# Kernel optimization log

Hardware: AMD Instinct MI355X
Metric: run time of the kernel (lower is better)

Reference implementation:

```python
import jax, jax.numpy as jnp
import numpy as np

B = 32768
PASSES = 4

# mask layout: (batch, digit, row, col), values in {0,1}

def _to_lines(m, d):
    """Reorder so the last axis enumerates the 9 cells of a line and axis -2 the 9 lines."""
    if d == 'h':
        return m                      # lines = rows, cells = cols
    if d == 'v':
        return jnp.swapaxes(m, 2, 3)  # lines = cols, cells = rows
    b = m.shape[0]                    # lines = 3x3 boxes
    return m.reshape(b, 9, 3, 3, 3, 3).transpose(0, 1, 2, 4, 3, 5).reshape(b, 9, 9, 9)

_from_lines = _to_lines  # all three reorderings are self-inverse


def filter_line(m, d):
    """SudokuFilterHVBox: remove a solved cell's digit from all other cells in its line."""
    l = _to_lines(m, d)
    cnt = l.sum(axis=1, keepdims=True)                 # candidates per cell
    solved = l * (cnt == 1).astype(l.dtype)            # one-hot solved cells
    other = solved.sum(axis=-1, keepdims=True) - solved  # same digit solved elsewhere in line
    out = l * (other == 0).astype(l.dtype)
    return _from_lines(out, d)


def unique_line(m, d):
    """SudokuUniqueHVBox (hidden single): if a digit fits only one cell in a line, fix it."""
    l = _to_lines(m, d)
    cnt_line = l.sum(axis=-1, keepdims=True)           # per-digit count in the line
    hidden = l * (cnt_line == 1).astype(l.dtype)       # lone placements
    has = hidden.sum(axis=1, keepdims=True) > 0        # cell hosts a hidden single
    out = jnp.where(has, hidden, l)
    return _from_lines(out, d)


def doubles_line(m, d):
    """SudokuDigitsDoubles (naked pair): two identical 2-candidate cells in a line
    eliminate those digits from the rest of the line."""
    l = _to_lines(m, d)                                # (B, d, line, cell)
    cnt = l.sum(axis=1, keepdims=True)
    pm = l * (cnt == 2).astype(l.dtype)                # patterns of 2-candidate cells
    dot = jnp.einsum('bdlc,bdle->blce', pm, pm)        # pattern overlap between cells
    eye = jnp.eye(9, dtype=l.dtype)
    match = (dot == 2).astype(l.dtype) * (1.0 - eye)   # identical pair at another cell
    pairflag = match.sum(-1) > 0                       # (B, line, cell) part of a naked pair
    pair_digit = pm * pairflag[:, None, :, :].astype(l.dtype)
    total_pd = pair_digit.sum(-1, keepdims=True)       # digit belongs to some pair in line
    remove = (total_pd > 0) & (pair_digit == 0)
    out = l * (1.0 - remove.astype(l.dtype))
    return _from_lines(out, d)


def pointing(m, d):
    """SudokuDigitsInOneLineAtBox: if a digit's box candidates lie in one row/col,
    remove that digit from the rest of the row/col outside the box."""
    b = m.shape[0]
    v = m.reshape(b, 9, 3, 3, 3, 3)                    # (B, d, br, ri, bc, ci)
    if d == 'h':
        pres = v.sum(axis=5) > 0                       # (B,d,br,ri,bc) digit in row of box
        nrows = pres.sum(axis=3, keepdims=True)
        point = pres & (nrows == 1)                    # confined to single row within box
        tot = point.sum(axis=4, keepdims=True)         # over bc
        rem = (tot - point) > 0                        # pointing from another box hits us
        out = v * (1.0 - rem[..., None].astype(v.dtype))
    else:
        pres = v.sum(axis=3) > 0                       # (B,d,br,bc,ci) digit in col of box
        ncols = pres.sum(axis=4, keepdims=True)
        point = pres & (ncols == 1)
        tot = point.sum(axis=2, keepdims=True)         # over br
        rem = (tot - point) > 0
        out = v * (1.0 - rem[:, :, :, None, :, :].astype(v.dtype))
    return out.reshape(b, 9, 9, 9)


def _forward_mask(mask):
    for _ in range(PASSES):
        mask = filter_line(mask, 'box')
        mask = pointing(mask, 'h')
        mask = pointing(mask, 'v')
        mask = unique_line(mask, 'h')
        mask = unique_line(mask, 'v')
        mask = unique_line(mask, 'box')
        mask = doubles_line(mask, 'v')   # original code instantiates doubles_h with 'v'
        mask = doubles_line(mask, 'v')
        mask = doubles_line(mask, 'box')
    return mask


def setup_inputs() -> dict:
    key = jax.random.key(0)
    mask = jax.random.randint(key, (B, 9, 9, 9), 0, 2).astype(jnp.float32)
    return {"mask": mask}


def reference(mask):
    out = _forward_mask(mask)
    cnt = out.sum(axis=1)                              # candidates per cell
    solved = jnp.all(cnt == 1, axis=(1, 2))            # (B,) puzzle fully determined
    return (out, solved)
```

## Files before the change

### kernel.cpp

```cpp
#include <hip/hip_runtime.h>
#include <stdint.h>

#define NB 32768
#define NPASS 4
#define FULL27 0x07FFFFFFu
#define NWORDS (NB * 27)


__global__ __launch_bounds__(256)
void pack_kernel(const uint32_t* __restrict__ in, uint32_t* __restrict__ packed) {
    __shared__ uint32_t pool[4][56];
    const int lane = threadIdx.x & 63;
    const int wv = threadIdx.x >> 6;
    const size_t wordBase = (size_t)blockIdx.x * 256 + (size_t)wv * 64;
    const uint32_t* src = in + wordBase * 27;
    #pragma unroll
    for (int i = 0; i < 27; ++i) {
        uint32_t v = src[(size_t)i * 64 + lane];
        unsigned long long m = __ballot(v != 0u);
        if (lane == 0) {
            pool[wv][2 * i]     = (uint32_t)m;
            pool[wv][2 * i + 1] = (uint32_t)(m >> 32);
        }
    }
    __syncthreads();
    const int bit = lane * 27;
    const int di = bit >> 5;
    uint64_t both = (uint64_t)pool[wv][di] | ((uint64_t)pool[wv][di + 1] << 32);
    packed[wordBase + lane] = (uint32_t)(both >> (bit & 31)) & FULL27;
}

__device__ __forceinline__ uint32_t colfold(uint32_t w) {
    return (w | (w >> 9) | (w >> 18)) & 0x1FFu;
}
__device__ __forceinline__ uint32_t colmaj2(uint32_t w) {
    return ((w & (w >> 9)) | ((w | (w >> 9)) & (w >> 18))) & 0x1FFu;
}

__global__ __launch_bounds__(192, 1)
void solve_kernel(const uint32_t* __restrict__ pin, uint32_t* __restrict__ pout,
                  float* __restrict__ solved) {
    __shared__ uint32_t exA[3][36][64];
    __shared__ uint32_t exB[3][9][64];
    const int lane = threadIdx.x & 63;
    const int band = threadIdx.x >> 6;
    const int bo1 = band == 2 ? 0 : band + 1;
    const int bo2 = band == 0 ? 2 : band - 1;
    const int p = blockIdx.x * 64 + lane;

    uint32_t bd[9];
    {
        const uint32_t* src = pin + (size_t)p * 27 + band;
        #pragma unroll
        for (int d = 0; d < 9; ++d) bd[d] = src[d * 3];
    }

    #pragma unroll 1
    for (int pass = 0; pass < NPASS; ++pass) {
        {
            uint32_t on = 0, tw = 0, fo = 0;
            #pragma unroll
            for (int d = 0; d < 9; ++d) {
                uint32_t c = on & bd[d];
                on ^= bd[d]; fo |= tw & c; tw ^= c;
            }
            uint32_t ex1 = on & ~tw & ~fo;
            #pragma unroll
            for (int d = 0; d < 9; ++d) {
                uint32_t s = bd[d] & ex1;
                #pragma unroll
                for (int k = 0; k < 3; ++k) {
                    uint32_t bm = 0x1C0E07u << (3 * k);
                    uint32_t sm = s & bm;
                    uint32_t multi = sm & (sm - 1u);
                    uint32_t keep = (sm == 0u) ? 0xFFFFFFFFu : (~bm | (multi ? 0u : sm));
                    bd[d] &= keep;
                }
            }
        }

        #pragma unroll
        for (int d = 0; d < 9; ++d) {
            uint32_t w = bd[d];
            uint32_t t = (w | (w >> 1) | (w >> 2)) & 0x01249249u;
            uint32_t sum = (t & 0x1FFu) + ((t >> 9) & 0x1FFu) + ((t >> 18) & 0x1FFu);
            uint32_t single = sum & ~(sum >> 1) & 0x49u;
            uint32_t point = t & (single * 0x40201u);
            uint32_t clearm = 0;
            #pragma unroll
            for (int r = 0; r < 3; ++r) {
                uint32_t pr = (point >> (9 * r)) & 0x1FFu;
                uint32_t multi = pr & (pr - 1u);
                uint32_t segkeep = multi ? 0u : pr * 7u;
                uint32_t rc = pr ? ((0x1FFu & ~segkeep) << (9 * r)) : 0u;
                clearm |= rc;
            }
            bd[d] = w & ~clearm;
        }

        #pragma unroll
        for (int d = 0; d < 9; ++d) {
            uint32_t w = bd[d];
            uint32_t q = colfold(w);
            uint32_t u = (q & 0x49u) + ((q >> 1) & 0x49u) + ((q >> 2) & 0x49u);
            uint32_t single = u & ~(u >> 1) & 0x49u;
            exA[band][d][lane] = q & (single * 7u);
        }
        __syncthreads();
        #pragma unroll
        for (int d = 0; d < 9; ++d) {
            uint32_t o = exA[bo1][d][lane] | exA[bo2][d][lane];
            bd[d] &= ~(o * 0x40201u);
        }

        {
            uint32_t hid[9], has = 0;
            #pragma unroll
            for (int d = 0; d < 9; ++d) {
                uint32_t w = bd[d], h = 0;
                #pragma unroll
                for (int r = 0; r < 3; ++r) {
                    uint32_t x = w & (0x1FFu << (9 * r));
                    h |= (x & (x - 1u)) ? 0u : x;
                }
                hid[d] = h; has |= h;
            }
            #pragma unroll
            for (int d = 0; d < 9; ++d) bd[d] = (bd[d] & ~has) | hid[d];
        }

        {
            #pragma unroll
            for (int d = 0; d < 9; ++d) {
                uint32_t w = bd[d];
                exB[band][d][lane] = colfold(w) | (colmaj2(w) << 9);
            }
            __syncthreads();
            uint32_t hid[9], has = 0;
            #pragma unroll
            for (int d = 0; d < 9; ++d) {
                uint32_t w = bd[d];
                uint32_t q0 = colfold(w), m0 = colmaj2(w);
                uint32_t ea = exB[bo1][d][lane], eb = exB[bo2][d][lane];
                uint32_t qa = ea & 0x1FFu, ma = ea >> 9;
                uint32_t qb = eb & 0x1FFu, mb = eb >> 9;
                uint32_t ge2 = m0 | ma | mb | (q0 & qa) | (q0 & qb) | (qa & qb);
                uint32_t ex1c = (q0 | qa | qb) & ~ge2;
                hid[d] = w & ((ex1c & q0) * 0x40201u);
                has |= hid[d];
            }
            #pragma unroll
            for (int d = 0; d < 9; ++d) bd[d] = (bd[d] & ~has) | hid[d];
        }

        {
            uint32_t hid[9], has = 0;
            #pragma unroll
            for (int d = 0; d < 9; ++d) {
                uint32_t w = bd[d], h = 0;
                #pragma unroll
                for (int k = 0; k < 3; ++k) {
                    uint32_t x = w & (0x1C0E07u << (3 * k));
                    h |= (x & (x - 1u)) ? 0u : x;
                }
                hid[d] = h; has |= h;
            }
            #pragma unroll
            for (int d = 0; d < 9; ++d) bd[d] = (bd[d] & ~has) | hid[d];
        }

        #pragma unroll 1
        for (int rep = 0; rep < 2; ++rep) {
            uint32_t on = 0, tw = 0, fo = 0;
            #pragma unroll
            for (int d = 0; d < 9; ++d) {
                uint32_t c = on & bd[d];
                on ^= bd[d]; fo |= tw & c; tw ^= c;
            }
            uint32_t ex2 = tw & ~on & ~fo;
            uint32_t Q[9], K[9];
            #pragma unroll
            for (int d = 0; d < 9; ++d) { Q[d] = bd[d] & ex2; K[d] = 0u; }
            {
                int s = 0;
                #pragma unroll
                for (int d1 = 0; d1 < 9; ++d1)
                    #pragma unroll
                    for (int d2 = d1 + 1; d2 < 9; ++d2) {
                        uint32_t P = Q[d1] & Q[d2];
                        exA[band][s][lane] = colfold(P) | (colmaj2(P) << 9);
                        ++s;
                    }
            }
            __syncthreads();
            {
                int s = 0;
                #pragma unroll
                for (int d1 = 0; d1 < 9; ++d1)
                    #pragma unroll
                    for (int d2 = d1 + 1; d2 < 9; ++d2) {
                        uint32_t P = Q[d1] & Q[d2];
                        uint32_t f0 = colfold(P), g0 = colmaj2(P);
                        uint32_t ea = exA[bo1][s][lane], eb = exA[bo2][s][lane];
                        uint32_t fa = ea & 0x1FFu, ga = ea >> 9;
                        uint32_t fb = eb & 0x1FFu, gb = eb >> 9;
                        uint32_t dup = g0 | ga | gb | (f0 & fa) | (f0 & fb) | (fa & fb);
                        uint32_t sK = P & (dup * 0x40201u);
                        K[d1] |= sK; K[d2] |= sK;
                        ++s;
                    }
            }
            #pragma unroll
            for (int d = 0; d < 9; ++d) exB[band][d][lane] = colfold(K[d]);
            __syncthreads();
            #pragma unroll
            for (int d = 0; d < 9; ++d) {
                uint32_t cols = colfold(K[d]) | exB[bo1][d][lane] | exB[bo2][d][lane];
                uint32_t em = cols * 0x40201u;
                bd[d] = (bd[d] & ~em) | K[d];
            }
        }

        {
            uint32_t on = 0, tw = 0, fo = 0;
            #pragma unroll
            for (int d = 0; d < 9; ++d) {
                uint32_t c = on & bd[d];
                on ^= bd[d]; fo |= tw & c; tw ^= c;
            }
            uint32_t ex2 = tw & ~on & ~fo;
            uint32_t Q[9], K[9];
            #pragma unroll
            for (int d = 0; d < 9; ++d) { Q[d] = bd[d] & ex2; K[d] = 0u; }
            #pragma unroll
            for (int d1 = 0; d1 < 9; ++d1)
                #pragma unroll
                for (int d2 = d1 + 1; d2 < 9; ++d2) {
                    uint32_t P = Q[d1] & Q[d2];
                    #pragma unroll
                    for (int k = 0; k < 3; ++k) {
                        uint32_t m = P & (0x1C0E07u << (3 * k));
                        uint32_t s = (m & (m - 1u)) ? m : 0u;
                        K[d1] |= s; K[d2] |= s;
                    }
                }
            #pragma unroll
            for (int d = 0; d < 9; ++d)
                #pragma unroll
                for (int k = 0; k < 3; ++k) {
                    uint32_t bm = 0x1C0E07u << (3 * k);
                    uint32_t t = K[d] & bm;
                    uint32_t mask = t ? (~bm | t) : 0xFFFFFFFFu;
                    bd[d] &= mask;
                }
        }
    }

    {
        uint32_t* dst = pout + (size_t)p * 27 + band;
        #pragma unroll
        for (int d = 0; d < 9; ++d) dst[d * 3] = bd[d];
    }
    {
        uint32_t on = 0, tw = 0, fo = 0;
        #pragma unroll
        for (int d = 0; d < 9; ++d) {
            uint32_t c = on & bd[d];
            on ^= bd[d]; fo |= tw & c; tw ^= c;
        }
        exA[band][0][lane] = ((on & ~tw & ~fo) == FULL27) ? 1u : 0u;
        __syncthreads();
        if (band == 0) {
            uint32_t all = exA[0][0][lane] & exA[1][0][lane] & exA[2][0][lane];
            solved[p] = all ? 1.0f : 0.0f;
        }
    }
}

__global__ __launch_bounds__(256)
void expand_kernel(const uint32_t* __restrict__ packed, float4* __restrict__ out4) {
    int tid = blockIdx.x * blockDim.x + threadIdx.x;
    int base = tid * 4;
    int w0 = (int)((unsigned)base / 27u);
    int pos0 = base - w0 * 27;
    uint32_t a = packed[w0];
    int w1 = w0 + 1; if (w1 > NWORDS - 1) w1 = NWORDS - 1;
    uint32_t b = packed[w1];
    float r[4];
    #pragma unroll
    for (int k = 0; k < 4; ++k) {
        int pp = pos0 + k;
        uint32_t word = (pp < 27) ? a : b;
        int sh = (pp < 27) ? pp : pp - 27;
        r[k] = (float)((word >> sh) & 1u);
    }
    out4[tid] = make_float4(r[0], r[1], r[2], r[3]);
}

extern "C" void kernel_launch(void* const* d_in, const int* in_sizes, int n_in,
                              void* d_out, int out_size, void* d_ws, size_t ws_size,
                              hipStream_t stream) {
    const uint32_t* in = (const uint32_t*)d_in[0];
    float* out = (float*)d_out;
    float* solved = out + (size_t)NB * 729;
    uint32_t* packed = (uint32_t*)d_ws;

    pack_kernel<<<NWORDS / 256, 256, 0, stream>>>(in, packed);
    solve_kernel<<<NB / 64, 192, 0, stream>>>(packed, packed, solved);
    expand_kernel<<<(NB * 729 / 4) / 256, 256, 0, stream>>>(packed, (float4*)out);
}
```

Before: 235.4 us.

## Co-locate a puzzle's three bands in one wavefront and exchange via shuffles

Remaps threads so the three band-threads of each puzzle are adjacent lanes within a single wavefront (21 puzzles per wave, 84 per block). All shared-memory exchanges and __syncthreads barriers are replaced by cross-lane __shfl reads, and the solved-flag reduction also moves to shuffles. One lane in every 64 is left idle and needs a validity guard, and each shuffle costs LDS-crossbar bandwidth, but block-wide barriers and LDS store/load pairs go away.

```diff
diff --git a/kernel.cpp b/kernel.cpp
--- a/kernel.cpp
+++ b/kernel.cpp
@@ -37,20 +37,24 @@
     return ((w & (w >> 9)) | ((w | (w >> 9)) & (w >> 18))) & 0x1FFu;
 }
 
-__global__ __launch_bounds__(192, 1)
+__global__ __launch_bounds__(256, 1)
 void solve_kernel(const uint32_t* __restrict__ pin, uint32_t* __restrict__ pout,
                   float* __restrict__ solved) {
-    __shared__ uint32_t exA[3][36][64];
-    __shared__ uint32_t exB[3][9][64];
     const int lane = threadIdx.x & 63;
-    const int band = threadIdx.x >> 6;
+    const int wv   = threadIdx.x >> 6;
+    const int trip = lane / 3;
+    const int band = lane - trip * 3;
     const int bo1 = band == 2 ? 0 : band + 1;
     const int bo2 = band == 0 ? 2 : band - 1;
-    const int p = blockIdx.x * 64 + lane;
+    int sl1 = trip * 3 + bo1; if (sl1 > 63) sl1 = 63;
+    int sl2 = trip * 3 + bo2; if (sl2 > 63) sl2 = 63;
+    const int p = blockIdx.x * 84 + wv * 21 + trip;
+    const bool valid = (trip < 21) && (p < NB);
+    const int pl = valid ? p : (NB - 1);
 
     uint32_t bd[9];
     {
-        const uint32_t* src = pin + (size_t)p * 27 + band;
+        const uint32_t* src = pin + (size_t)pl * 27 + band;
         #pragma unroll
         for (int d = 0; d < 9; ++d) bd[d] = src[d * 3];
     }
@@ -98,19 +102,22 @@
             bd[d] = w & ~clearm;
         }
 
-        #pragma unroll
-        for (int d = 0; d < 9; ++d) {
-            uint32_t w = bd[d];
-            uint32_t q = colfold(w);
-            uint32_t u = (q & 0x49u) + ((q >> 1) & 0x49u) + ((q >> 2) & 0x49u);
-            uint32_t single = u & ~(u >> 1) & 0x49u;
-            exA[band][d][lane] = q & (single * 7u);
-        }
-        __syncthreads();
-        #pragma unroll
-        for (int d = 0; d < 9; ++d) {
-            uint32_t o = exA[bo1][d][lane] | exA[bo2][d][lane];
-            bd[d] &= ~(o * 0x40201u);
+        {
+            uint32_t pnt[9];
+            #pragma unroll
+            for (int d = 0; d < 9; ++d) {
+                uint32_t w = bd[d];
+                uint32_t q = colfold(w);
+                uint32_t u = (q & 0x49u) + ((q >> 1) & 0x49u) + ((q >> 2) & 0x49u);
+                uint32_t single = u & ~(u >> 1) & 0x49u;
+                pnt[d] = q & (single * 7u);
+            }
+            #pragma unroll
+            for (int d = 0; d < 9; ++d) {
+                uint32_t o = (uint32_t)__shfl((int)pnt[d], sl1, 64) |
+                             (uint32_t)__shfl((int)pnt[d], sl2, 64);
+                bd[d] &= ~(o * 0x40201u);
+            }
         }
 
         {
@@ -130,18 +137,14 @@
         }
 
         {
-            #pragma unroll
-            for (int d = 0; d < 9; ++d) {
-                uint32_t w = bd[d];
-                exB[band][d][lane] = colfold(w) | (colmaj2(w) << 9);
-            }
-            __syncthreads();
             uint32_t hid[9], has = 0;
             #pragma unroll
             for (int d = 0; d < 9; ++d) {
                 uint32_t w = bd[d];
                 uint32_t q0 = colfold(w), m0 = colmaj2(w);
-                uint32_t ea = exB[bo1][d][lane], eb = exB[bo2][d][lane];
+                uint32_t ex = q0 | (m0 << 9);
+                uint32_t ea = (uint32_t)__shfl((int)ex, sl1, 64);
+                uint32_t eb = (uint32_t)__shfl((int)ex, sl2, 64);
                 uint32_t qa = ea & 0x1FFu, ma = ea >> 9;
                 uint32_t qb = eb & 0x1FFu, mb = eb >> 9;
                 uint32_t ge2 = m0 | ma | mb | (q0 & qa) | (q0 & qb) | (qa & qb);
@@ -181,41 +184,26 @@
             uint32_t Q[9], K[9];
             #pragma unroll
             for (int d = 0; d < 9; ++d) { Q[d] = bd[d] & ex2; K[d] = 0u; }
-            {
-                int s = 0;
-                #pragma unroll
-                for (int d1 = 0; d1 < 9; ++d1)
-                    #pragma unroll
-                    for (int d2 = d1 + 1; d2 < 9; ++d2) {
-                        uint32_t P = Q[d1] & Q[d2];
-                        exA[band][s][lane] = colfold(P) | (colmaj2(P) << 9);
-                        ++s;
-                    }
-            }
-            __syncthreads();
-            {
-                int s = 0;
-                #pragma unroll
-                for (int d1 = 0; d1 < 9; ++d1)
-                    #pragma unroll
-                    for (int d2 = d1 + 1; d2 < 9; ++d2) {
-                        uint32_t P = Q[d1] & Q[d2];
-                        uint32_t f0 = colfold(P), g0 = colmaj2(P);
-                        uint32_t ea = exA[bo1][s][lane], eb = exA[bo2][s][lane];
-                        uint32_t fa = ea & 0x1FFu, ga = ea >> 9;
-                        uint32_t fb = eb & 0x1FFu, gb = eb >> 9;
-                        uint32_t dup = g0 | ga | gb | (f0 & fa) | (f0 & fb) | (fa & fb);
-                        uint32_t sK = P & (dup * 0x40201u);
-                        K[d1] |= sK; K[d2] |= sK;
-                        ++s;
-                    }
-            }
-            #pragma unroll
-            for (int d = 0; d < 9; ++d) exB[band][d][lane] = colfold(K[d]);
-            __syncthreads();
-            #pragma unroll
-            for (int d = 0; d < 9; ++d) {
-                uint32_t cols = colfold(K[d]) | exB[bo1][d][lane] | exB[bo2][d][lane];
+            #pragma unroll
+            for (int d1 = 0; d1 < 9; ++d1)
+                #pragma unroll
+                for (int d2 = d1 + 1; d2 < 9; ++d2) {
+                    uint32_t P = Q[d1] & Q[d2];
+                    uint32_t f0 = colfold(P), g0 = colmaj2(P);
+                    uint32_t ex = f0 | (g0 << 9);
+                    uint32_t ea = (uint32_t)__shfl((int)ex, sl1, 64);
+                    uint32_t eb = (uint32_t)__shfl((int)ex, sl2, 64);
+                    uint32_t fa = ea & 0x1FFu, ga = ea >> 9;
+                    uint32_t fb = eb & 0x1FFu, gb = eb >> 9;
+                    uint32_t dup = g0 | ga | gb | (f0 & fa) | (f0 & fb) | (fa & fb);
+                    uint32_t sK = P & (dup * 0x40201u);
+                    K[d1] |= sK; K[d2] |= sK;
+                }
+            #pragma unroll
+            for (int d = 0; d < 9; ++d) {
+                uint32_t kc = colfold(K[d]);
+                uint32_t cols = kc | (uint32_t)__shfl((int)kc, sl1, 64)
+                                   | (uint32_t)__shfl((int)kc, sl2, 64);
                 uint32_t em = cols * 0x40201u;
                 bd[d] = (bd[d] & ~em) | K[d];
             }
@@ -256,7 +244,7 @@
         }
     }
 
-    {
+    if (valid) {
         uint32_t* dst = pout + (size_t)p * 27 + band;
         #pragma unroll
         for (int d = 0; d < 9; ++d) dst[d * 3] = bd[d];
@@ -268,12 +256,10 @@
             uint32_t c = on & bd[d];
             on ^= bd[d]; fo |= tw & c; tw ^= c;
         }
-        exA[band][0][lane] = ((on & ~tw & ~fo) == FULL27) ? 1u : 0u;
-        __syncthreads();
-        if (band == 0) {
-            uint32_t all = exA[0][0][lane] & exA[1][0][lane] & exA[2][0][lane];
-            solved[p] = all ? 1.0f : 0.0f;
-        }
+        uint32_t okb = ((on & ~tw & ~fo) == FULL27) ? 1u : 0u;
+        uint32_t all = okb & (uint32_t)__shfl((int)okb, sl1, 64)
+                           & (uint32_t)__shfl((int)okb, sl2, 64);
+        if (valid && band == 0) solved[p] = all ? 1.0f : 0.0f;
     }
 }
 
@@ -306,6 +292,6 @@
     uint32_t* packed = (uint32_t*)d_ws;
 
     pack_kernel<<<NWORDS / 256, 256, 0, stream>>>(in, packed);
-    solve_kernel<<<NB / 64, 192, 0, stream>>>(packed, packed, solved);
+    solve_kernel<<<(NB + 83) / 84, 256, 0, stream>>>(packed, packed, solved);
     expand_kernel<<<(NB * 729 / 4) / 256, 256, 0, stream>>>(packed, (float4*)out);
 }
```

Measured after the change: 235.4 us. Within noise of the previous version (+0.0%).
